# Kernel tuning notes

Measured on AMD Instinct MI355X. Metric: run time of the kernel, lower is better.

Reference implementation:

```python
import jax, jax.numpy as jnp
import numpy as np

DN = ('NCHW', 'OIHW', 'NCHW')

def binarize(t):
    # torch: t.sign().add(0.5).sign() -> +1 for t>=0 (incl. 0), -1 for t<0
    return jnp.where(t >= 0, jnp.float32(1.0), jnp.float32(-1.0)).astype(t.dtype)

def bconv(x, w, b, dil):
    # weights binarized to +/-1 (as in BinaryConv2d), bias stays float
    wb = binarize(w)
    y = jax.lax.conv_general_dilated(
        x, wb, window_strides=(1, 1), padding='SAME',
        rhs_dilation=(dil, dil), dimension_numbers=DN)
    return y + b[None, :, None, None]

def prelu(x, a):
    return jnp.where(x >= 0, x, a[0] * x)

def setup_inputs() -> dict:
    key = jax.random.key(0)
    ks = jax.random.split(key, 12)
    C, Cq = 256, 64
    B, H, W = 8, 128, 128
    inp = {
        'x':  jax.random.normal(ks[0], (B, C, H, W), dtype=jnp.float32),
        'w1': jax.random.normal(ks[1], (Cq, C, 1, 5), dtype=jnp.float32) * 0.05,
        'b1': jax.random.normal(ks[2], (Cq,), dtype=jnp.float32) * 0.05,
        'w2': jax.random.normal(ks[3], (Cq, C, 1, 5), dtype=jnp.float32) * 0.05,
        'b2': jax.random.normal(ks[4], (Cq,), dtype=jnp.float32) * 0.05,
        'w3': jax.random.normal(ks[5], (Cq, C, 5, 1), dtype=jnp.float32) * 0.05,
        'b3': jax.random.normal(ks[6], (Cq,), dtype=jnp.float32) * 0.05,
        'w4': jax.random.normal(ks[7], (Cq, C, 5, 1), dtype=jnp.float32) * 0.05,
        'b4': jax.random.normal(ks[8], (Cq,), dtype=jnp.float32) * 0.05,
        'a1': jnp.full((1,), 0.25, dtype=jnp.float32),  # PReLU default init
        'wc': jax.random.normal(ks[9], (C, C, 3, 3), dtype=jnp.float32) * 0.05,
        'bc': jax.random.normal(ks[10], (C,), dtype=jnp.float32) * 0.05,
        'a2': jnp.full((1,), 0.25, dtype=jnp.float32),
    }
    return inp

def reference(x, w1, b1, w2, b2, w3, b3, w4, b4, a1, wc, bc, a2):
    out = binarize(x)
    # MrbConv2d: four +/-1 weight branches, channel-concat
    o1 = bconv(out, w1, b1, 1)   # (1,5) dil 1
    o2 = bconv(out, w2, b2, 2)   # (1,5) dil 2
    o3 = bconv(out, w3, b3, 1)   # (5,1) dil 1
    o4 = bconv(out, w4, b4, 2)   # (5,1) dil 2
    out = jnp.concatenate([o1, o2, o3, o4], axis=1)
    out = prelu(out, a1)
    out = binarize(out)
    out = bconv(out, wc, bc, 1)  # (3,3) dil 1
    out = prelu(out, a2)
    return out + x
```

## Files before the change

kernel.cpp:

```cpp
#include <hip/hip_runtime.h>
#include <cstdint>


#define HWD 128
#define NB  8

__global__ __launch_bounds__(256) void pack_x(const float* __restrict__ x,
                                              uint32_t* __restrict__ xb) {
  int id = blockIdx.x * 256 + threadIdx.x;
  int w  = id & 127;
  int wd = (id >> 7) & 7;
  int h  = (id >> 10) & 127;
  int n  = id >> 17;
  const float* src = x + ((n * 256 + wd * 32) << 14) + (h << 7) + w;
  uint32_t bits = 0;
#pragma unroll
  for (int i = 0; i < 32; ++i) {
    float v = src[i << 14];
    bits |= (v < 0.0f ? 1u : 0u) << i;
  }
  xb[(((((n << 7) + h) << 7) + w) << 3) + wd] = bits;
}

__global__ __launch_bounds__(256) void pack_w(
    const float* __restrict__ w1, const float* __restrict__ w2,
    const float* __restrict__ w3, const float* __restrict__ w4,
    const float* __restrict__ wc,
    const float* __restrict__ b1, const float* __restrict__ b2,
    const float* __restrict__ b3, const float* __restrict__ b4,
    uint32_t* __restrict__ wl1, uint32_t* __restrict__ wl2,
    float* __restrict__ bcat) {
  int id = blockIdx.x * 256 + threadIdx.x;
  if (id < 10240) {
    int wd  = id & 7;
    int tap = (id >> 3) % 5;
    int oc  = (id / 40) & 63;
    int br  = id / 2560;
    const float* w = (br == 0) ? w1 : (br == 1) ? w2 : (br == 2) ? w3 : w4;
    uint32_t bits = 0;
#pragma unroll
    for (int i = 0; i < 32; ++i) {
      float v = w[(oc * 256 + wd * 32 + i) * 5 + tap];
      bits |= (v < 0.0f ? 1u : 0u) << i;
    }
    wl1[id] = bits;
  } else if (id < 28672) {
    int id2 = id - 10240;
    int wd  = id2 & 7;
    int tap = (id2 >> 3) % 9;
    int oc  = id2 / 72;
    uint32_t bits = 0;
#pragma unroll
    for (int i = 0; i < 32; ++i) {
      float v = wc[(oc * 256 + wd * 32 + i) * 9 + tap];
      bits |= (v < 0.0f ? 1u : 0u) << i;
    }
    wl2[id2] = bits;
  } else if (id < 28928) {
    int c = id - 28672;
    float v = (c < 64) ? b1[c] : (c < 128) ? b2[c - 64]
              : (c < 192) ? b3[c - 128] : b4[c - 192];
    bcat[c] = v;
  }
}

__global__ __launch_bounds__(256) void layer1(
    const uint32_t* __restrict__ xb, uint32_t* __restrict__ yb,
    const uint32_t* __restrict__ wl1, const float* __restrict__ bcat,
    const float* __restrict__ a1p) {
  __shared__ uint32_t lw[10240];
  __shared__ float lb[256];
  const int t = threadIdx.x;
  {
    const uint4* wsrc = (const uint4*)wl1;
    uint4* ldst = (uint4*)lw;
#pragma unroll
    for (int k = 0; k < 10; ++k) ldst[t + 256 * k] = wsrc[t + 256 * k];
    lb[t] = bcat[t];
  }
  __syncthreads();
  const float a1 = a1p[0];
  int p = blockIdx.x * 256 + t;
  int w = p & 127, h = (p >> 7) & 127, n = p >> 14;

  uint32_t outw[8];
#pragma unroll
  for (int br = 0; br < 4; ++br) {
    uint4 ia[5], ib[5];
    int msk[5];
    int nval = 0;
#pragma unroll
    for (int tap = 0; tap < 5; ++tap) {
      int dh = 0, dw = 0;
      if (br == 0) dw = tap - 2;
      else if (br == 1) dw = 2 * tap - 4;
      else if (br == 2) dh = tap - 2;
      else dh = 2 * tap - 4;
      int hh = h + dh, ww = w + dw;
      bool v = (hh >= 0) && (hh < HWD) && (ww >= 0) && (ww < HWD);
      msk[tap] = v ? -1 : 0;
      nval += v ? 1 : 0;
      int hc = min(max(hh, 0), HWD - 1), wc2 = min(max(ww, 0), HWD - 1);
      const uint4* src = (const uint4*)(xb + (((((n << 7) + hc) << 7) + wc2) << 3));
      ia[tap] = src[0];
      ib[tap] = src[1];
    }
    int basev = 256 * nval;
    uint32_t bits[2];
#pragma unroll
    for (int half = 0; half < 2; ++half) {
      uint32_t bw = 0;
      for (int oc = 0; oc < 32; ++oc) {
        int ocg = half * 32 + oc;
        const uint4* wp = (const uint4*)(lw + (br * 64 + ocg) * 40);
        int acc = 0;
#pragma unroll
        for (int tap = 0; tap < 5; ++tap) {
          uint4 wa = wp[tap * 2], wb = wp[tap * 2 + 1];
          int ta = __popc(ia[tap].x ^ wa.x) + __popc(ia[tap].y ^ wa.y) +
                   __popc(ia[tap].z ^ wa.z) + __popc(ia[tap].w ^ wa.w) +
                   __popc(ib[tap].x ^ wb.x) + __popc(ib[tap].y ^ wb.y) +
                   __popc(ib[tap].z ^ wb.z) + __popc(ib[tap].w ^ wb.w);
          acc += ta & msk[tap];
        }
        float v = (float)(basev - 2 * acc) + lb[br * 64 + ocg];
        v = v >= 0.0f ? v : a1 * v;
        bw |= (v < 0.0f ? 1u : 0u) << oc;
      }
      bits[half] = bw;
    }
    outw[br * 2] = bits[0];
    outw[br * 2 + 1] = bits[1];
  }
  uint4* dst = (uint4*)(yb + (p << 3));
  dst[0] = make_uint4(outw[0], outw[1], outw[2], outw[3]);
  dst[1] = make_uint4(outw[4], outw[5], outw[6], outw[7]);
}

__global__ __launch_bounds__(256) void layer2(
    const uint32_t* __restrict__ yb, const uint32_t* __restrict__ wl2,
    const float* __restrict__ bc, const float* __restrict__ a2p,
    const float* __restrict__ x, float* __restrict__ out) {
  __shared__ uint32_t lw[9216];
  __shared__ float lb[256];
  const int t = threadIdx.x;
  lb[t] = bc[t];
  const float a2 = a2p[0];
  int p = blockIdx.x * 256 + t;
  int w = p & 127, h = (p >> 7) & 127, n = p >> 14;

  uint4 ia[9], ib[9];
  int msk[9];
  int nval = 0;
#pragma unroll
  for (int ky = 0; ky < 3; ++ky) {
#pragma unroll
    for (int kx = 0; kx < 3; ++kx) {
      int tap = ky * 3 + kx;
      int hh = h + ky - 1, ww = w + kx - 1;
      bool v = (hh >= 0) && (hh < HWD) && (ww >= 0) && (ww < HWD);
      msk[tap] = v ? -1 : 0;
      nval += v ? 1 : 0;
      int hc = min(max(hh, 0), HWD - 1), wc2 = min(max(ww, 0), HWD - 1);
      const uint4* src = (const uint4*)(yb + (((((n << 7) + hc) << 7) + wc2) << 3));
      ia[tap] = src[0];
      ib[tap] = src[1];
    }
  }
  int basev = 256 * nval;
  const float* xs = x + (n << 22) + (h << 7) + w;
  float* os = out + (n << 22) + (h << 7) + w;

  for (int ch = 0; ch < 2; ++ch) {
    __syncthreads();
    {
      const uint4* wsrc = (const uint4*)(wl2 + ch * 9216);
      uint4* ldst = (uint4*)lw;
#pragma unroll
      for (int k = 0; k < 9; ++k) ldst[t + 256 * k] = wsrc[t + 256 * k];
    }
    __syncthreads();
    for (int oc = 0; oc < 128; ++oc) {
      int ocg = ch * 128 + oc;
      const uint4* wp = (const uint4*)(lw + oc * 72);
      int acc = 0;
#pragma unroll
      for (int tap = 0; tap < 9; ++tap) {
        uint4 wa = wp[tap * 2], wb = wp[tap * 2 + 1];
        int ta = __popc(ia[tap].x ^ wa.x) + __popc(ia[tap].y ^ wa.y) +
                 __popc(ia[tap].z ^ wa.z) + __popc(ia[tap].w ^ wa.w) +
                 __popc(ib[tap].x ^ wb.x) + __popc(ib[tap].y ^ wb.y) +
                 __popc(ib[tap].z ^ wb.z) + __popc(ib[tap].w ^ wb.w);
        acc += ta & msk[tap];
      }
      float v = (float)(basev - 2 * acc) + lb[ocg];
      v = v >= 0.0f ? v : a2 * v;
      os[ocg << 14] = v + xs[ocg << 14];
    }
  }
}

extern "C" void kernel_launch(void* const* d_in, const int* in_sizes, int n_in,
                              void* d_out, int out_size, void* d_ws, size_t ws_size,
                              hipStream_t stream) {
  const float* x  = (const float*)d_in[0];
  const float* w1 = (const float*)d_in[1];
  const float* b1 = (const float*)d_in[2];
  const float* w2 = (const float*)d_in[3];
  const float* b2 = (const float*)d_in[4];
  const float* w3 = (const float*)d_in[5];
  const float* b3 = (const float*)d_in[6];
  const float* w4 = (const float*)d_in[7];
  const float* b4 = (const float*)d_in[8];
  const float* a1 = (const float*)d_in[9];
  const float* wc = (const float*)d_in[10];
  const float* bc = (const float*)d_in[11];
  const float* a2 = (const float*)d_in[12];
  float* out = (float*)d_out;

  uint32_t* ws  = (uint32_t*)d_ws;
  uint32_t* xb  = ws;
  uint32_t* yb  = ws + (1 << 20);
  uint32_t* wl1 = ws + (2 << 20);
  uint32_t* wl2 = wl1 + 10240;
  float*    bcat = (float*)(wl2 + 18432);

  pack_x<<<4096, 256, 0, stream>>>(x, xb);
  pack_w<<<113, 256, 0, stream>>>(w1, w2, w3, w4, wc, b1, b2, b3, b4, wl1, wl2, bcat);
  layer1<<<512, 256, 0, stream>>>(xb, yb, wl1, bcat, a1);
  layer2<<<512, 256, 0, stream>>>(yb, wl2, bc, a2, x, out);
}
```

Baseline: 613.1 us.

## Split layers across branch/channel blocks, drop border masks with separate fixup kernels

Layer1 and layer2 now launch 4x more blocks, each handling one branch or one 64-channel chunk, so less shared memory is used per block and occupancy rises. The interior kernels assume every tap is valid and clamp coordinates without masking, and border pixels are then recomputed correctly by new small fixup kernels. pack_x reads float4 vectors and packs four pixels per thread. In exchange there are extra launches, xb/yb are reloaded once per branch or chunk, and correctness depends on the fixup kernels running after the main kernels.

```diff
diff --git a/kernel.cpp b/kernel.cpp
--- a/kernel.cpp
+++ b/kernel.cpp
@@ -3,23 +3,29 @@
 
 
 #define HWD 128
-#define NB  8
 
 __global__ __launch_bounds__(256) void pack_x(const float* __restrict__ x,
                                               uint32_t* __restrict__ xb) {
   int id = blockIdx.x * 256 + threadIdx.x;
-  int w  = id & 127;
-  int wd = (id >> 7) & 7;
-  int h  = (id >> 10) & 127;
-  int n  = id >> 17;
-  const float* src = x + ((n * 256 + wd * 32) << 14) + (h << 7) + w;
-  uint32_t bits = 0;
-#pragma unroll
-  for (int i = 0; i < 32; ++i) {
-    float v = src[i << 14];
-    bits |= (v < 0.0f ? 1u : 0u) << i;
-  }
-  xb[(((((n << 7) + h) << 7) + w) << 3) + wd] = bits;
+  int w4 = id & 31;
+  int wd = (id >> 5) & 7;
+  int h  = (id >> 8) & 127;
+  int n  = id >> 15;
+  const float4* src = (const float4*)(x + ((n * 256 + wd * 32) << 14) + (h << 7) + (w4 << 2));
+  uint32_t b0 = 0, b1 = 0, b2 = 0, b3 = 0;
+#pragma unroll
+  for (int c = 0; c < 32; ++c) {
+    float4 v = src[c << 12];
+    b0 |= (v.x < 0.0f ? 1u : 0u) << c;
+    b1 |= (v.y < 0.0f ? 1u : 0u) << c;
+    b2 |= (v.z < 0.0f ? 1u : 0u) << c;
+    b3 |= (v.w < 0.0f ? 1u : 0u) << c;
+  }
+  int p0 = (n << 14) + (h << 7) + (w4 << 2);
+  xb[((p0 + 0) << 3) + wd] = b0;
+  xb[((p0 + 1) << 3) + wd] = b1;
+  xb[((p0 + 2) << 3) + wd] = b2;
+  xb[((p0 + 3) << 3) + wd] = b3;
 }
 
 __global__ __launch_bounds__(256) void pack_w(
@@ -64,128 +70,107 @@
   }
 }
 
-__global__ __launch_bounds__(256) void layer1(
+__global__ __launch_bounds__(256) void layer1_main(
     const uint32_t* __restrict__ xb, uint32_t* __restrict__ yb,
     const uint32_t* __restrict__ wl1, const float* __restrict__ bcat,
     const float* __restrict__ a1p) {
-  __shared__ uint32_t lw[10240];
-  __shared__ float lb[256];
-  const int t = threadIdx.x;
+  __shared__ uint32_t lw[2560];
+  __shared__ float lb[64];
+  const int br = blockIdx.x >> 9;
+  const int pb = blockIdx.x & 511;
+  const int t  = threadIdx.x;
   {
-    const uint4* wsrc = (const uint4*)wl1;
+    const uint4* wsrc = (const uint4*)(wl1 + br * 2560);
     uint4* ldst = (uint4*)lw;
-#pragma unroll
-    for (int k = 0; k < 10; ++k) ldst[t + 256 * k] = wsrc[t + 256 * k];
-    lb[t] = bcat[t];
+    for (int k = t; k < 640; k += 256) ldst[k] = wsrc[k];
+    if (t < 64) lb[t] = bcat[br * 64 + t];
   }
   __syncthreads();
   const float a1 = a1p[0];
-  int p = blockIdx.x * 256 + t;
+  int p = pb * 256 + t;
   int w = p & 127, h = (p >> 7) & 127, n = p >> 14;
-
-  uint32_t outw[8];
-#pragma unroll
-  for (int br = 0; br < 4; ++br) {
-    uint4 ia[5], ib[5];
-    int msk[5];
-    int nval = 0;
-#pragma unroll
-    for (int tap = 0; tap < 5; ++tap) {
-      int dh = 0, dw = 0;
-      if (br == 0) dw = tap - 2;
-      else if (br == 1) dw = 2 * tap - 4;
-      else if (br == 2) dh = tap - 2;
-      else dh = 2 * tap - 4;
-      int hh = h + dh, ww = w + dw;
-      bool v = (hh >= 0) && (hh < HWD) && (ww >= 0) && (ww < HWD);
-      msk[tap] = v ? -1 : 0;
-      nval += v ? 1 : 0;
-      int hc = min(max(hh, 0), HWD - 1), wc2 = min(max(ww, 0), HWD - 1);
-      const uint4* src = (const uint4*)(xb + (((((n << 7) + hc) << 7) + wc2) << 3));
-      ia[tap] = src[0];
-      ib[tap] = src[1];
-    }
-    int basev = 256 * nval;
-    uint32_t bits[2];
-#pragma unroll
-    for (int half = 0; half < 2; ++half) {
-      uint32_t bw = 0;
-      for (int oc = 0; oc < 32; ++oc) {
-        int ocg = half * 32 + oc;
-        const uint4* wp = (const uint4*)(lw + (br * 64 + ocg) * 40);
-        int acc = 0;
-#pragma unroll
-        for (int tap = 0; tap < 5; ++tap) {
-          uint4 wa = wp[tap * 2], wb = wp[tap * 2 + 1];
-          int ta = __popc(ia[tap].x ^ wa.x) + __popc(ia[tap].y ^ wa.y) +
-                   __popc(ia[tap].z ^ wa.z) + __popc(ia[tap].w ^ wa.w) +
-                   __popc(ib[tap].x ^ wb.x) + __popc(ib[tap].y ^ wb.y) +
-                   __popc(ib[tap].z ^ wb.z) + __popc(ib[tap].w ^ wb.w);
-          acc += ta & msk[tap];
-        }
-        float v = (float)(basev - 2 * acc) + lb[br * 64 + ocg];
-        v = v >= 0.0f ? v : a1 * v;
-        bw |= (v < 0.0f ? 1u : 0u) << oc;
+  const int dil = (br & 1) ? 2 : 1;
+  const bool horiz = (br < 2);
+
+  uint4 ia[5], ib[5];
+#pragma unroll
+  for (int tap = 0; tap < 5; ++tap) {
+    int d = dil * (tap - 2);
+    int hh = horiz ? h : min(max(h + d, 0), HWD - 1);
+    int ww = horiz ? min(max(w + d, 0), HWD - 1) : w;
+    const uint4* src = (const uint4*)(xb + (((((n << 7) + hh) << 7) + ww) << 3));
+    ia[tap] = src[0];
+    ib[tap] = src[1];
+  }
+
+  uint32_t bw[2];
+#pragma unroll
+  for (int half = 0; half < 2; ++half) {
+    uint32_t b = 0;
+    for (int oc = 0; oc < 32; ++oc) {
+      const uint4* wp = (const uint4*)(lw + (half * 32 + oc) * 40);
+      int acc = 0;
+#pragma unroll
+      for (int tap = 0; tap < 5; ++tap) {
+        uint4 wa = wp[tap * 2], wb = wp[tap * 2 + 1];
+        acc = __popc(ia[tap].x ^ wa.x) + acc;
+        acc = __popc(ia[tap].y ^ wa.y) + acc;
+        acc = __popc(ia[tap].z ^ wa.z) + acc;
+        acc = __popc(ia[tap].w ^ wa.w) + acc;
+        acc = __popc(ib[tap].x ^ wb.x) + acc;
+        acc = __popc(ib[tap].y ^ wb.y) + acc;
+        acc = __popc(ib[tap].z ^ wb.z) + acc;
+        acc = __popc(ib[tap].w ^ wb.w) + acc;
       }
-      bits[half] = bw;
-    }
-    outw[br * 2] = bits[0];
-    outw[br * 2 + 1] = bits[1];
-  }
-  uint4* dst = (uint4*)(yb + (p << 3));
-  dst[0] = make_uint4(outw[0], outw[1], outw[2], outw[3]);
-  dst[1] = make_uint4(outw[4], outw[5], outw[6], outw[7]);
-}
-
-__global__ __launch_bounds__(256) void layer2(
-    const uint32_t* __restrict__ yb, const uint32_t* __restrict__ wl2,
-    const float* __restrict__ bc, const float* __restrict__ a2p,
-    const float* __restrict__ x, float* __restrict__ out) {
-  __shared__ uint32_t lw[9216];
-  __shared__ float lb[256];
-  const int t = threadIdx.x;
-  lb[t] = bc[t];
-  const float a2 = a2p[0];
-  int p = blockIdx.x * 256 + t;
-  int w = p & 127, h = (p >> 7) & 127, n = p >> 14;
-
-  uint4 ia[9], ib[9];
-  int msk[9];
-  int nval = 0;
-#pragma unroll
-  for (int ky = 0; ky < 3; ++ky) {
-#pragma unroll
-    for (int kx = 0; kx < 3; ++kx) {
-      int tap = ky * 3 + kx;
-      int hh = h + ky - 1, ww = w + kx - 1;
-      bool v = (hh >= 0) && (hh < HWD) && (ww >= 0) && (ww < HWD);
-      msk[tap] = v ? -1 : 0;
-      nval += v ? 1 : 0;
-      int hc = min(max(hh, 0), HWD - 1), wc2 = min(max(ww, 0), HWD - 1);
-      const uint4* src = (const uint4*)(yb + (((((n << 7) + hc) << 7) + wc2) << 3));
-      ia[tap] = src[0];
-      ib[tap] = src[1];
-    }
+      float v = (float)(1280 - 2 * acc) + lb[half * 32 + oc];
+      v = v >= 0.0f ? v : a1 * v;
+      b |= (v < 0.0f ? 1u : 0u) << oc;
+    }
+    bw[half] = b;
+  }
+  *(uint2*)(yb + (p << 3) + br * 2) = make_uint2(bw[0], bw[1]);
+}
+
+__global__ __launch_bounds__(256) void layer1_fix(
+    const uint32_t* __restrict__ xb, uint32_t* __restrict__ yb,
+    const uint32_t* __restrict__ wl1, const float* __restrict__ bcat,
+    const float* __restrict__ a1p) {
+  int id = blockIdx.x * 256 + threadIdx.x;
+  int br  = id >> 13;
+  int rem = id & 8191;
+  int e  = rem & 7;
+  int e2 = (e < 4) ? e : 120 + e;
+  int o  = (rem >> 3) & 127;
+  int n  = rem >> 10;
+  int w, h;
+  if (br < 2) { w = e2; h = o; } else { h = e2; w = o; }
+  const int dil = (br & 1) ? 2 : 1;
+  const bool horiz = (br < 2);
+  const float a1 = a1p[0];
+
+  uint4 ia[5], ib[5];
+  int msk[5]; int nval = 0;
+#pragma unroll
+  for (int tap = 0; tap < 5; ++tap) {
+    int d = dil * (tap - 2);
+    int hh = horiz ? h : h + d;
+    int ww = horiz ? w + d : w;
+    bool v = (hh >= 0) && (hh < HWD) && (ww >= 0) && (ww < HWD);
+    msk[tap] = v ? -1 : 0; nval += v ? 1 : 0;
+    int hc = min(max(hh, 0), HWD - 1), wc2 = min(max(ww, 0), HWD - 1);
+    const uint4* src = (const uint4*)(xb + (((((n << 7) + hc) << 7) + wc2) << 3));
+    ia[tap] = src[0]; ib[tap] = src[1];
   }
   int basev = 256 * nval;
-  const float* xs = x + (n << 22) + (h << 7) + w;
-  float* os = out + (n << 22) + (h << 7) + w;
-
-  for (int ch = 0; ch < 2; ++ch) {
-    __syncthreads();
-    {
-      const uint4* wsrc = (const uint4*)(wl2 + ch * 9216);
-      uint4* ldst = (uint4*)lw;
-#pragma unroll
-      for (int k = 0; k < 9; ++k) ldst[t + 256 * k] = wsrc[t + 256 * k];
-    }
-    __syncthreads();
-    for (int oc = 0; oc < 128; ++oc) {
-      int ocg = ch * 128 + oc;
-      const uint4* wp = (const uint4*)(lw + oc * 72);
+  uint32_t bw[2];
+#pragma unroll
+  for (int half = 0; half < 2; ++half) {
+    uint32_t b = 0;
+    for (int oc = 0; oc < 32; ++oc) {
+      const uint4* wp = (const uint4*)(wl1 + (br * 64 + half * 32 + oc) * 40);
       int acc = 0;
 #pragma unroll
-      for (int tap = 0; tap < 9; ++tap) {
+      for (int tap = 0; tap < 5; ++tap) {
         uint4 wa = wp[tap * 2], wb = wp[tap * 2 + 1];
         int ta = __popc(ia[tap].x ^ wa.x) + __popc(ia[tap].y ^ wa.y) +
                  __popc(ia[tap].z ^ wa.z) + __popc(ia[tap].w ^ wa.w) +
@@ -193,10 +178,122 @@
                  __popc(ib[tap].z ^ wb.z) + __popc(ib[tap].w ^ wb.w);
         acc += ta & msk[tap];
       }
-      float v = (float)(basev - 2 * acc) + lb[ocg];
-      v = v >= 0.0f ? v : a2 * v;
-      os[ocg << 14] = v + xs[ocg << 14];
-    }
+      float v = (float)(basev - 2 * acc) + bcat[br * 64 + half * 32 + oc];
+      v = v >= 0.0f ? v : a1 * v;
+      b |= (v < 0.0f ? 1u : 0u) << oc;
+    }
+    bw[half] = b;
+  }
+  int p = (n << 14) + (h << 7) + w;
+  *(uint2*)(yb + (p << 3) + br * 2) = make_uint2(bw[0], bw[1]);
+}
+
+__global__ __launch_bounds__(256) void layer2_main(
+    const uint32_t* __restrict__ yb, const uint32_t* __restrict__ wl2,
+    const float* __restrict__ bc, const float* __restrict__ a2p,
+    const float* __restrict__ x, float* __restrict__ out) {
+  __shared__ uint32_t lw[4608];
+  __shared__ float lb[64];
+  const int ch = blockIdx.x >> 9;
+  const int pb = blockIdx.x & 511;
+  const int t  = threadIdx.x;
+  {
+    const uint4* wsrc = (const uint4*)(wl2 + ch * 4608);
+    uint4* ldst = (uint4*)lw;
+    for (int k = t; k < 1152; k += 256) ldst[k] = wsrc[k];
+    if (t < 64) lb[t] = bc[ch * 64 + t];
+  }
+  __syncthreads();
+  const float a2 = a2p[0];
+  int p = pb * 256 + t;
+  int w = p & 127, h = (p >> 7) & 127, n = p >> 14;
+
+  uint4 ia[9], ib[9];
+#pragma unroll
+  for (int ky = 0; ky < 3; ++ky) {
+#pragma unroll
+    for (int kx = 0; kx < 3; ++kx) {
+      int tap = ky * 3 + kx;
+      int hh = min(max(h + ky - 1, 0), HWD - 1);
+      int ww = min(max(w + kx - 1, 0), HWD - 1);
+      const uint4* src = (const uint4*)(yb + (((((n << 7) + hh) << 7) + ww) << 3));
+      ia[tap] = src[0]; ib[tap] = src[1];
+    }
+  }
+  const float* xs = x + (n << 22) + (ch << 20) + (h << 7) + w;
+  float* os = out + (n << 22) + (ch << 20) + (h << 7) + w;
+
+  for (int oc = 0; oc < 64; ++oc) {
+    const uint4* wp = (const uint4*)(lw + oc * 72);
+    int acc = 0;
+#pragma unroll
+    for (int tap = 0; tap < 9; ++tap) {
+      uint4 wa = wp[tap * 2], wb = wp[tap * 2 + 1];
+      acc = __popc(ia[tap].x ^ wa.x) + acc;
+      acc = __popc(ia[tap].y ^ wa.y) + acc;
+      acc = __popc(ia[tap].z ^ wa.z) + acc;
+      acc = __popc(ia[tap].w ^ wa.w) + acc;
+      acc = __popc(ib[tap].x ^ wb.x) + acc;
+      acc = __popc(ib[tap].y ^ wb.y) + acc;
+      acc = __popc(ib[tap].z ^ wb.z) + acc;
+      acc = __popc(ib[tap].w ^ wb.w) + acc;
+    }
+    float v = (float)(2304 - 2 * acc) + lb[oc];
+    v = v >= 0.0f ? v : a2 * v;
+    os[oc << 14] = v + xs[oc << 14];
+  }
+}
+
+__global__ __launch_bounds__(256) void layer2_fix(
+    const uint32_t* __restrict__ yb, const uint32_t* __restrict__ wl2,
+    const float* __restrict__ bc, const float* __restrict__ a2p,
+    const float* __restrict__ x, float* __restrict__ out) {
+  int id = blockIdx.x * 256 + threadIdx.x;
+  int chunk = id >> 12;
+  int k = id & 4095;
+  if (k >= 4064) return;
+  int n = k / 508, r = k % 508;
+  int h, w;
+  if (r < 128)      { h = 0;   w = r; }
+  else if (r < 256) { h = 127; w = r - 128; }
+  else if (r < 382) { w = 0;   h = r - 255; }
+  else              { w = 127; h = r - 381; }
+  const float a2 = a2p[0];
+
+  uint4 ia[9], ib[9];
+  int msk[9]; int nval = 0;
+#pragma unroll
+  for (int ky = 0; ky < 3; ++ky) {
+#pragma unroll
+    for (int kx = 0; kx < 3; ++kx) {
+      int tap = ky * 3 + kx;
+      int hh = h + ky - 1, ww = w + kx - 1;
+      bool v = (hh >= 0) && (hh < HWD) && (ww >= 0) && (ww < HWD);
+      msk[tap] = v ? -1 : 0; nval += v ? 1 : 0;
+      int hc = min(max(hh, 0), HWD - 1), wc2 = min(max(ww, 0), HWD - 1);
+      const uint4* src = (const uint4*)(yb + (((((n << 7) + hc) << 7) + wc2) << 3));
+      ia[tap] = src[0]; ib[tap] = src[1];
+    }
+  }
+  int basev = 256 * nval;
+  const float* xs = x + (n << 22) + (h << 7) + w;
+  float* os = out + (n << 22) + (h << 7) + w;
+  for (int oc = 0; oc < 32; ++oc) {
+    int ocg = chunk * 32 + oc;
+    const uint4* wp = (const uint4*)(wl2 + ocg * 72);
+    int acc = 0;
+#pragma unroll
+    for (int tap = 0; tap < 9; ++tap) {
+      uint4 wa = wp[tap * 2], wb = wp[tap * 2 + 1];
+      int ta = __popc(ia[tap].x ^ wa.x) + __popc(ia[tap].y ^ wa.y) +
+               __popc(ia[tap].z ^ wa.z) + __popc(ia[tap].w ^ wa.w) +
+               __popc(ib[tap].x ^ wb.x) + __popc(ib[tap].y ^ wb.y) +
+               __popc(ib[tap].z ^ wb.z) + __popc(ib[tap].w ^ wb.w);
+      acc += ta & msk[tap];
+    }
+    float v = (float)(basev - 2 * acc) + bc[ocg];
+    v = v >= 0.0f ? v : a2 * v;
+    os[ocg << 14] = v + xs[ocg << 14];
   }
 }
 
@@ -225,8 +322,10 @@
   uint32_t* wl2 = wl1 + 10240;
   float*    bcat = (float*)(wl2 + 18432);
 
-  pack_x<<<4096, 256, 0, stream>>>(x, xb);
+  pack_x<<<1024, 256, 0, stream>>>(x, xb);
   pack_w<<<113, 256, 0, stream>>>(w1, w2, w3, w4, wc, b1, b2, b3, b4, wl1, wl2, bcat);
-  layer1<<<512, 256, 0, stream>>>(xb, yb, wl1, bcat, a1);
-  layer2<<<512, 256, 0, stream>>>(yb, wl2, bc, a2, x, out);
-}
+  layer1_main<<<2048, 256, 0, stream>>>(xb, yb, wl1, bcat, a1);
+  layer1_fix<<<128, 256, 0, stream>>>(xb, yb, wl1, bcat, a1);
+  layer2_main<<<2048, 256, 0, stream>>>(yb, wl2, bc, a2, x, out);
+  layer2_fix<<<128, 256, 0, stream>>>(yb, wl2, bc, a2, x, out);
+}
```

Result: slower. 666.2 us (+8.7%).
